# Optimization experiments

Hardware: AMD Instinct MI355X
Metric: run time of the kernel (lower is better)

## Reference

```python
import jax, jax.numpy as jnp
import numpy as np

B, D, C, K = 8192, 2048, 4096, 1000  # batch, input_dim, num_centers, num_classes


def setup_inputs() -> dict:
    key = jax.random.key(0)
    k0, k1, k2 = jax.random.split(key, 3)
    x = jax.random.normal(k0, (B, D), dtype=jnp.float32)
    centers = jax.random.normal(k1, (C, D), dtype=jnp.float32)
    beta = jnp.ones((C,), dtype=jnp.float32)
    W = jax.random.normal(k2, (K, C), dtype=jnp.float32) * 0.02  # fc.weight
    b = jnp.zeros((K,), dtype=jnp.float32)  # fc.bias
    return {"x": x, "centers": centers, "beta": beta, "W": W, "b": b}


def reference(x, centers, beta, W, b):
    # Pairwise Euclidean distance via the Gram trick (same math as
    # torch.norm(x[:,None,:] - centers, dim=2), without the (B,C,D) intermediate).
    x2 = jnp.sum(x * x, axis=-1, keepdims=True)          # (B, 1)
    c2 = jnp.sum(centers * centers, axis=-1)             # (C,)
    sq = x2 + c2[None, :] - 2.0 * (x @ centers.T)        # (B, C) squared distances
    dist = jnp.sqrt(jnp.maximum(sq, 0.0))
    act = jnp.exp(-beta[None, :] * dist)                 # RBF activations
    act = act / jnp.sum(act, axis=1, keepdims=True)      # normalize over centers
    return act @ W.T + b                                 # linear head (B, K)
```

## Files before the change

### kernel.cpp

```cpp
#include <hip/hip_runtime.h>


#define BB 8192
#define DD 2048
#define CC 4096
#define KK 1000
#define KP 1024

typedef unsigned short u16;
typedef __bf16 bf16x8 __attribute__((ext_vector_type(8)));
typedef float f32x4 __attribute__((ext_vector_type(4)));

typedef const void __attribute__((address_space(1)))* gvp_t;
typedef void __attribute__((address_space(3)))* lvp_t;

__device__ __forceinline__ u16 f2bf(float f) {
  union { float f; unsigned u; } v; v.f = f;
  return (u16)((v.u + 0x7fffu + ((v.u >> 16) & 1u)) >> 16);
}

__global__ void prep_all(const float* __restrict__ x, const float* __restrict__ cen,
                         const float* __restrict__ W,
                         u16* __restrict__ xb, u16* __restrict__ cb,
                         u16* __restrict__ wb,
                         float* __restrict__ x2, float* __restrict__ c2) {
  int row = blockIdx.x;
  int t = threadIdx.x;
  if (row >= BB + CC) {
    int r = row - BB - CC;
    ushort4* dst = reinterpret_cast<ushort4*>(wb + (size_t)r * CC);
    if (r < KK) {
      const float4* src = reinterpret_cast<const float4*>(W + (size_t)r * CC);
#pragma unroll
      for (int m = 0; m < 4; ++m) {
        float4 v = src[t + 256 * m];
        dst[t + 256 * m] = make_ushort4(f2bf(v.x), f2bf(v.y), f2bf(v.z), f2bf(v.w));
      }
    } else {
#pragma unroll
      for (int m = 0; m < 4; ++m) dst[t + 256 * m] = make_ushort4(0, 0, 0, 0);
    }
    return;
  }
  const float* src;
  u16* dst;
  float* nrm;
  if (row < BB) {
    src = x + (size_t)row * DD; dst = xb + (size_t)row * DD; nrm = x2 + row;
  } else {
    int r = row - BB;
    src = cen + (size_t)r * DD; dst = cb + (size_t)r * DD; nrm = c2 + r;
  }
  float s = 0.f;
#pragma unroll
  for (int m = 0; m < 2; ++m) {
    int idx = t + 256 * m;
    float4 v = reinterpret_cast<const float4*>(src)[idx];
    s += v.x * v.x + v.y * v.y + v.z * v.z + v.w * v.w;
    reinterpret_cast<ushort4*>(dst)[idx] =
        make_ushort4(f2bf(v.x), f2bf(v.y), f2bf(v.z), f2bf(v.w));
  }
#pragma unroll
  for (int off = 1; off < 64; off <<= 1) s += __shfl_xor(s, off);
  __shared__ float red[4];
  if ((t & 63) == 0) red[t >> 6] = s;
  __syncthreads();
  if (t == 0) *nrm = red[0] + red[1] + red[2] + red[3];
}

#define SB0 __builtin_amdgcn_sched_barrier(0)
#define BARR __builtin_amdgcn_s_barrier()
#define LGKM0 asm volatile("s_waitcnt lgkmcnt(0)" ::: "memory")


#define ST_A(BUF, H, TILE)                                                         \
  {                                                                                \
    const u16* _s = gA0 + (size_t)((H) * 128) * DD + (TILE) * 64;                  \
    char* _d = (char*)smem + (BUF) * 65536 + (H) * 16384 + t * 16;                 \
    __builtin_amdgcn_global_load_lds((gvp_t)_s, (lvp_t)_d, 16, 0, 0);              \
    __builtin_amdgcn_global_load_lds((gvp_t)(_s + (size_t)64 * DD),                \
                                     (lvp_t)(_d + 8192), 16, 0, 0);                \
  }

#define ST_B(BUF, H, TILE)                                                         \
  {                                                                                \
    const u16* _s = gB0 + (size_t)((H) * 128) * DD + (TILE) * 64;                  \
    char* _d = (char*)smem + (BUF) * 65536 + 32768 + (H) * 16384 + t * 16;         \
    __builtin_amdgcn_global_load_lds((gvp_t)_s, (lvp_t)_d, 16, 0, 0);              \
    __builtin_amdgcn_global_load_lds((gvp_t)(_s + (size_t)64 * DD),                \
                                     (lvp_t)(_d + 8192), 16, 0, 0);                \
  }

#define READ_B(SBP)                                                                \
  _Pragma("unroll") for (int n_ = 0; n_ < 4; ++n_) {                               \
    _Pragma("unroll") for (int ks_ = 0; ks_ < 2; ++ks_) {                          \
      bfr[n_][ks_] = *(const bf16x8*)((SBP) + bRow + n_ * 2048 + cbv[ks_]);        \
    }                                                                              \
  }

#define READ_A(SAP, MQ)                                                            \
  _Pragma("unroll") for (int m_ = 0; m_ < 2; ++m_) {                               \
    _Pragma("unroll") for (int ks_ = 0; ks_ < 2; ++ks_) {                          \
      af[m_][ks_] =                                                                \
          *(const bf16x8*)((SAP) + aRow + ((MQ)*2 + m_) * 2048 + cbv[ks_]);        \
    }                                                                              \
  }

#define MFMA_Q(MQ)                                                                 \
  __builtin_amdgcn_s_setprio(1);                                                   \
  _Pragma("unroll") for (int m_ = 0; m_ < 2; ++m_) {                               \
    _Pragma("unroll") for (int n_ = 0; n_ < 4; ++n_) {                             \
      _Pragma("unroll") for (int ks_ = 0; ks_ < 2; ++ks_) {                        \
        acc[(MQ)*2 + m_][n_] = __builtin_amdgcn_mfma_f32_16x16x32_bf16(            \
            af[m_][ks_], bfr[n_][ks_], acc[(MQ)*2 + m_][n_], 0, 0, 0);             \
      }                                                                            \
    }                                                                              \
  }                                                                                \
  __builtin_amdgcn_s_setprio(0)

#define TILE_BODY(TILE, CUR, DOA, DOB, VMN)                                        \
  {                                                                                \
    const char* sA_ = (const char*)smem + (CUR) * 65536;                           \
    const char* sB_ = sA_ + 32768;                                                 \
    READ_B(sB_);                                                                   \
    READ_A(sA_, 0);                                                                \
    SB0;                                                                           \
    if (DOA) { ST_A(1 - (CUR), 0, (TILE) + 1); ST_A(1 - (CUR), 1, (TILE) + 1); }   \
    SB0; LGKM0; SB0;                                                               \
    MFMA_Q(0); SB0; BARR;                                                          \
    READ_A(sA_, 1); SB0;                                                           \
    if (DOB) { ST_B((CUR), 0, (TILE) + 2); }                                       \
    SB0; LGKM0; SB0;                                                               \
    MFMA_Q(1); SB0;                                                                \
    READ_A(sA_, 2); SB0;                                                           \
    if (DOB) { ST_B((CUR), 1, (TILE) + 2); }                                       \
    SB0; LGKM0; SB0;                                                               \
    MFMA_Q(2); SB0;                                                                \
    READ_A(sA_, 3); SB0; LGKM0; SB0;                                               \
    MFMA_Q(3);                                                                     \
    if ((VMN) == 4) { asm volatile("s_waitcnt vmcnt(4)" ::: "memory"); }           \
    else if ((VMN) == 0) { asm volatile("s_waitcnt vmcnt(0)" ::: "memory"); }      \
    SB0; BARR;                                                                     \
  }

__global__ __launch_bounds__(512, 2)
void gemm1_rbf(const u16* __restrict__ Abf, const u16* __restrict__ Bbf,
               const float* __restrict__ x2, const float* __restrict__ c2,
               const float* __restrict__ beta, u16* __restrict__ Ebf,
               float* __restrict__ psum) {
  constexpr int NT = DD / 64;
  __shared__ __align__(16) char smem[131072];

  const int t = threadIdx.x;
  const int lane = t & 63;
  const int wave = t >> 6;
  const int wr = wave >> 2;
  const int wc = wave & 3;
  const int l15 = lane & 15;

  const int rowBase = blockIdx.y * 256;
  const int colBase = blockIdx.x * 256;

  f32x4 acc[8][4];
#pragma unroll
  for (int i = 0; i < 8; ++i)
#pragma unroll
    for (int j = 0; j < 4; ++j) acc[i][j] = 0.f;

  const int srow = t >> 3;
  const u16* gA0 = Abf + (size_t)(rowBase + srow) * DD + ((t & 7) ^ (srow & 7)) * 8;
  const u16* gB0 = Bbf + (size_t)(colBase + srow) * DD + ((t & 7) ^ (srow & 7)) * 8;

  int cbv[2];
  cbv[0] = (((lane >> 4) & 3) ^ (lane & 7)) << 4;
  cbv[1] = ((4 + ((lane >> 4) & 3)) ^ (lane & 7)) << 4;
  const int aRow = (wr * 128 + l15) * 128;
  const int bRow = (wc * 64 + l15) * 128;

  bf16x8 bfr[4][2];
  bf16x8 af[2][2];

  ST_A(0, 0, 0); ST_A(0, 1, 0); ST_B(0, 0, 0); ST_B(0, 1, 0);
  ST_B(1, 0, 1); ST_B(1, 1, 1);
  asm volatile("s_waitcnt vmcnt(4)" ::: "memory");
  BARR;

#pragma unroll 2
  for (int tile = 0; tile < NT - 2; ++tile) {
    TILE_BODY(tile, tile & 1, true, true, 4);
  }
  TILE_BODY(NT - 2, (NT - 2) & 1, true, false, 0);
  TILE_BODY(NT - 1, (NT - 1) & 1, false, false, -1);

  const int khi4 = (lane >> 4) * 4;
  float* lrs = (float*)smem;
  float c2v[4], bet[4];
  int gc[4];
#pragma unroll
  for (int n = 0; n < 4; ++n) {
    gc[n] = colBase + wc * 64 + n * 16 + l15;
    c2v[n] = c2[gc[n]];
    bet[n] = beta[gc[n]];
  }
#pragma unroll
  for (int m = 0; m < 8; ++m) {
#pragma unroll
    for (int r = 0; r < 4; ++r) {
      const int rrel = wr * 128 + m * 16 + khi4 + r;
      const int grow = rowBase + rrel;
      const float x2v = x2[grow];
      u16* orow = Ebf + (size_t)grow * CC;
      float rs = 0.f;
#pragma unroll
      for (int n = 0; n < 4; ++n) {
        float d = acc[m][n][r];
        float sq = fmaxf(x2v + c2v[n] - 2.0f * d, 0.0f);
        float e = __expf(-bet[n] * __builtin_amdgcn_sqrtf(sq));
        rs += e;
        orow[gc[n]] = f2bf(e);
      }
      lrs[rrel * 68 + wc * 16 + l15] = rs;
    }
  }
  __syncthreads();
  if (t < 256) {
    const f32x4* p = (const f32x4*)(lrs + t * 68);
    float s = 0.f;
#pragma unroll
    for (int i = 0; i < 16; ++i) {
      f32x4 v = p[i];
      s += v[0] + v[1] + v[2] + v[3];
    }
    psum[(size_t)blockIdx.x * BB + rowBase + t] = s;
  }
}

__global__ void rowsum_reduce(const float* __restrict__ psum, float* __restrict__ rowsum) {
  const int row = blockIdx.x * 256 + threadIdx.x;
  float s = 0.f;
#pragma unroll
  for (int b = 0; b < 16; ++b) s += psum[(size_t)b * BB + row];
  rowsum[row] = s;
}


#define ST2_A(BUF, H, TILE)                                                        \
  {                                                                                \
    const u16* _s = gA0 + (size_t)((H) * 128) * CC + (TILE) * 64;                  \
    char* _d = (char*)smem + (BUF) * 49152 + (H) * 16384 + t * 16;                 \
    __builtin_amdgcn_global_load_lds((gvp_t)_s, (lvp_t)_d, 16, 0, 0);              \
    __builtin_amdgcn_global_load_lds((gvp_t)(_s + (size_t)64 * CC),                \
                                     (lvp_t)(_d + 8192), 16, 0, 0);                \
  }

#define ST2_B(BUF, TILE)                                                           \
  {                                                                                \
    const u16* _s = gB0 + (TILE) * 64;                                             \
    char* _d = (char*)smem + (BUF) * 49152 + 32768 + t * 16;                       \
    __builtin_amdgcn_global_load_lds((gvp_t)_s, (lvp_t)_d, 16, 0, 0);              \
    __builtin_amdgcn_global_load_lds((gvp_t)(_s + (size_t)64 * CC),                \
                                     (lvp_t)(_d + 8192), 16, 0, 0);                \
  }

#define READ2_B(SBP)                                                               \
  _Pragma("unroll") for (int n_ = 0; n_ < 2; ++n_) {                               \
    _Pragma("unroll") for (int ks_ = 0; ks_ < 2; ++ks_) {                          \
      bfr[n_][ks_] = *(const bf16x8*)((SBP) + bRow + n_ * 2048 + cbv[ks_]);        \
    }                                                                              \
  }

#define READ2_A(SAP, MQ)                                                           \
  _Pragma("unroll") for (int m_ = 0; m_ < 2; ++m_) {                               \
    _Pragma("unroll") for (int ks_ = 0; ks_ < 2; ++ks_) {                          \
      af[m_][ks_] =                                                                \
          *(const bf16x8*)((SAP) + aRow + ((MQ)*2 + m_) * 2048 + cbv[ks_]);        \
    }                                                                              \
  }

#define MFMA2_Q(MQ)                                                                \
  __builtin_amdgcn_s_setprio(1);                                                   \
  _Pragma("unroll") for (int m_ = 0; m_ < 2; ++m_) {                               \
    _Pragma("unroll") for (int n_ = 0; n_ < 2; ++n_) {                             \
      _Pragma("unroll") for (int ks_ = 0; ks_ < 2; ++ks_) {                        \
        acc[(MQ)*2 + m_][n_] = __builtin_amdgcn_mfma_f32_16x16x32_bf16(            \
            af[m_][ks_], bfr[n_][ks_], acc[(MQ)*2 + m_][n_], 0, 0, 0);             \
      }                                                                            \
    }                                                                              \
  }                                                                                \
  __builtin_amdgcn_s_setprio(0)

#define TILE2_BODY(TILE, CUR, DOA, DOB, VMN)                                       \
  {                                                                                \
    const char* sA_ = (const char*)smem + (CUR) * 49152;                           \
    const char* sB_ = sA_ + 32768;                                                 \
    READ2_B(sB_);                                                                  \
    READ2_A(sA_, 0);                                                               \
    SB0;                                                                           \
    if (DOA) { ST2_A(1 - (CUR), 0, (TILE) + 1); }                                  \
    SB0; LGKM0; SB0;                                                               \
    MFMA2_Q(0); SB0; BARR;                                                         \
    READ2_A(sA_, 1); SB0;                                                          \
    if (DOA) { ST2_A(1 - (CUR), 1, (TILE) + 1); }                                  \
    SB0; LGKM0; SB0;                                                               \
    MFMA2_Q(1); SB0;                                                               \
    READ2_A(sA_, 2); SB0;                                                          \
    if (DOB) { ST2_B((CUR), (TILE) + 2); }                                         \
    SB0; LGKM0; SB0;                                                               \
    MFMA2_Q(2); SB0;                                                               \
    READ2_A(sA_, 3); SB0; LGKM0; SB0;                                              \
    MFMA2_Q(3);                                                                    \
    if ((VMN) == 2) { asm volatile("s_waitcnt vmcnt(2)" ::: "memory"); }           \
    else if ((VMN) == 0) { asm volatile("s_waitcnt vmcnt(0)" ::: "memory"); }      \
    SB0; BARR;                                                                     \
  }

__global__ __launch_bounds__(512, 2)
void gemm2_out(const u16* __restrict__ Ebf, const u16* __restrict__ Wbf,
               const float* __restrict__ rowsum, const float* __restrict__ bias,
               float* __restrict__ out) {
  constexpr int NT = CC / 64;
  __shared__ __align__(16) char smem[98304];

  const int t = threadIdx.x;
  const int lane = t & 63;
  const int wave = t >> 6;
  const int wr = wave >> 2;
  const int wc = wave & 3;
  const int l15 = lane & 15;

  const int d = blockIdx.x + (blockIdx.y << 3);
  const int s_ = d >> 3;
  const int by = (d & 7) + ((s_ >> 3) << 3);
  const int bx = s_ & 7;

  const int rowBase = by * 256;
  const int colBase = bx * 128;

  f32x4 acc[8][2];
#pragma unroll
  for (int i = 0; i < 8; ++i)
#pragma unroll
    for (int j = 0; j < 2; ++j) acc[i][j] = 0.f;

  const int srow = t >> 3;
  const u16* gA0 = Ebf + (size_t)(rowBase + srow) * CC + ((t & 7) ^ (srow & 7)) * 8;
  const u16* gB0 = Wbf + (size_t)(colBase + srow) * CC + ((t & 7) ^ (srow & 7)) * 8;

  int cbv[2];
  cbv[0] = (((lane >> 4) & 3) ^ (lane & 7)) << 4;
  cbv[1] = ((4 + ((lane >> 4) & 3)) ^ (lane & 7)) << 4;
  const int aRow = (wr * 128 + l15) * 128;
  const int bRow = (wc * 32 + l15) * 128;

  bf16x8 bfr[2][2];
  bf16x8 af[2][2];

  ST2_A(0, 0, 0); ST2_A(0, 1, 0); ST2_B(0, 0);
  ST2_B(1, 1);
  asm volatile("s_waitcnt vmcnt(2)" ::: "memory");
  BARR;

#pragma unroll 2
  for (int tile = 0; tile < NT - 2; ++tile) {
    TILE2_BODY(tile, tile & 1, true, true, 2);
  }
  TILE2_BODY(NT - 2, (NT - 2) & 1, true, false, 0);
  TILE2_BODY(NT - 1, (NT - 1) & 1, false, false, -1);

  const int khi4 = (lane >> 4) * 4;
  int gc[2];
  float bv[2];
#pragma unroll
  for (int n = 0; n < 2; ++n) {
    gc[n] = colBase + wc * 32 + n * 16 + l15;
    bv[n] = (gc[n] < KK) ? bias[gc[n]] : 0.f;
  }
#pragma unroll
  for (int m = 0; m < 8; ++m) {
#pragma unroll
    for (int r = 0; r < 4; ++r) {
      const int grow = rowBase + wr * 128 + m * 16 + khi4 + r;
      const float inv = 1.0f / rowsum[grow];
#pragma unroll
      for (int n = 0; n < 2; ++n) {
        if (gc[n] < KK)
          out[(size_t)grow * KK + gc[n]] = acc[m][n][r] * inv + bv[n];
      }
    }
  }
}

#define OFF_XB 0u
#define OFF_CB 33554432u
#define OFF_WB 50331648u
#define OFF_EB 58720256u
#define OFF_X2 125829120u
#define OFF_C2 125861888u
#define OFF_RS 125878272u

extern "C" void kernel_launch(void* const* d_in, const int* in_sizes, int n_in,
                              void* d_out, int out_size, void* d_ws, size_t ws_size,
                              hipStream_t stream) {
  const float* x = (const float*)d_in[0];
  const float* cen = (const float*)d_in[1];
  const float* beta = (const float*)d_in[2];
  const float* W = (const float*)d_in[3];
  const float* bias = (const float*)d_in[4];
  float* out = (float*)d_out;
  char* ws = (char*)d_ws;

  u16* xb = (u16*)(ws + OFF_XB);
  u16* cb = (u16*)(ws + OFF_CB);
  u16* wb = (u16*)(ws + OFF_WB);
  u16* eb = (u16*)(ws + OFF_EB);
  float* x2 = (float*)(ws + OFF_X2);
  float* c2 = (float*)(ws + OFF_C2);
  float* rowsum = (float*)(ws + OFF_RS);
  float* psum = out;

  prep_all<<<BB + CC + KP, 256, 0, stream>>>(x, cen, W, xb, cb, wb, x2, c2);
  gemm1_rbf<<<dim3(CC / 256, BB / 256), 512, 0, stream>>>(xb, cb, x2, c2, beta, eb, psum);
  rowsum_reduce<<<BB / 256, 256, 0, stream>>>(psum, rowsum);
  gemm2_out<<<dim3(KP / 128, BB / 256), 512, 0, stream>>>(eb, wb, rowsum, bias, out);
}
```

Measured before the change: 337.6 us.

## Simplify GEMM prefetch to one-tile-ahead and double-buffer A fragments

Both GEMM main loops are restructured. Previously, B tiles were prefetched two tiles ahead into the current buffer, which needed a barrier in the middle of each tile. Now A and B for the next tile are issued together at the start of each tile into the other buffer, leaving one barrier per tile. A fragment reads are ping-ponged between two register sets so the next quarter's LDS reads overlap the current quarter's MFMAs. The trade-off is a shorter prefetch distance for B, a full vmcnt(0) wait at the end of every tile, and more VGPR usage.

```diff
diff --git a/kernel.cpp b/kernel.cpp
--- a/kernel.cpp
+++ b/kernel.cpp
@@ -71,6 +71,7 @@
 #define SB0 __builtin_amdgcn_sched_barrier(0)
 #define BARR __builtin_amdgcn_s_barrier()
 #define LGKM0 asm volatile("s_waitcnt lgkmcnt(0)" ::: "memory")
+#define VM0 asm volatile("s_waitcnt vmcnt(0)" ::: "memory")
 
 
 #define ST_A(BUF, H, TILE)                                                         \
@@ -98,48 +99,46 @@
     }                                                                              \
   }
 
-#define READ_A(SAP, MQ)                                                            \
+#define READ_AF(DST, SAP, MQ)                                                      \
   _Pragma("unroll") for (int m_ = 0; m_ < 2; ++m_) {                               \
     _Pragma("unroll") for (int ks_ = 0; ks_ < 2; ++ks_) {                          \
-      af[m_][ks_] =                                                                \
+      DST[m_][ks_] =                                                               \
           *(const bf16x8*)((SAP) + aRow + ((MQ)*2 + m_) * 2048 + cbv[ks_]);        \
     }                                                                              \
   }
 
-#define MFMA_Q(MQ)                                                                 \
+#define MFMA_QF(SRC, MQ)                                                           \
   __builtin_amdgcn_s_setprio(1);                                                   \
   _Pragma("unroll") for (int m_ = 0; m_ < 2; ++m_) {                               \
     _Pragma("unroll") for (int n_ = 0; n_ < 4; ++n_) {                             \
       _Pragma("unroll") for (int ks_ = 0; ks_ < 2; ++ks_) {                        \
         acc[(MQ)*2 + m_][n_] = __builtin_amdgcn_mfma_f32_16x16x32_bf16(            \
-            af[m_][ks_], bfr[n_][ks_], acc[(MQ)*2 + m_][n_], 0, 0, 0);             \
+            SRC[m_][ks_], bfr[n_][ks_], acc[(MQ)*2 + m_][n_], 0, 0, 0);            \
       }                                                                            \
     }                                                                              \
   }                                                                                \
   __builtin_amdgcn_s_setprio(0)
 
-#define TILE_BODY(TILE, CUR, DOA, DOB, VMN)                                        \
+#define TILE_BODY(TILE, CUR, DOS)                                                  \
   {                                                                                \
     const char* sA_ = (const char*)smem + (CUR) * 65536;                           \
     const char* sB_ = sA_ + 32768;                                                 \
     READ_B(sB_);                                                                   \
-    READ_A(sA_, 0);                                                                \
+    READ_AF(af0, sA_, 0);                                                          \
     SB0;                                                                           \
-    if (DOA) { ST_A(1 - (CUR), 0, (TILE) + 1); ST_A(1 - (CUR), 1, (TILE) + 1); }   \
+    if (DOS) {                                                                     \
+      ST_A(1 - (CUR), 0, (TILE) + 1); ST_A(1 - (CUR), 1, (TILE) + 1);              \
+      ST_B(1 - (CUR), 0, (TILE) + 1); ST_B(1 - (CUR), 1, (TILE) + 1);              \
+    }                                                                              \
     SB0; LGKM0; SB0;                                                               \
-    MFMA_Q(0); SB0; BARR;                                                          \
-    READ_A(sA_, 1); SB0;                                                           \
-    if (DOB) { ST_B((CUR), 0, (TILE) + 2); }                                       \
-    SB0; LGKM0; SB0;                                                               \
-    MFMA_Q(1); SB0;                                                                \
-    READ_A(sA_, 2); SB0;                                                           \
-    if (DOB) { ST_B((CUR), 1, (TILE) + 2); }                                       \
-    SB0; LGKM0; SB0;                                                               \
-    MFMA_Q(2); SB0;                                                                \
-    READ_A(sA_, 3); SB0; LGKM0; SB0;                                               \
-    MFMA_Q(3);                                                                     \
-    if ((VMN) == 4) { asm volatile("s_waitcnt vmcnt(4)" ::: "memory"); }           \
-    else if ((VMN) == 0) { asm volatile("s_waitcnt vmcnt(0)" ::: "memory"); }      \
+    READ_AF(af1, sA_, 1); SB0;                                                     \
+    MFMA_QF(af0, 0); SB0; LGKM0; SB0;                                              \
+    READ_AF(af0, sA_, 2); SB0;                                                     \
+    MFMA_QF(af1, 1); SB0; LGKM0; SB0;                                              \
+    READ_AF(af1, sA_, 3); SB0;                                                     \
+    MFMA_QF(af0, 2); SB0; LGKM0; SB0;                                              \
+    MFMA_QF(af1, 3);                                                               \
+    if (DOS) { VM0; }                                                              \
     SB0; BARR;                                                                     \
   }
 
@@ -178,19 +177,17 @@
   const int bRow = (wc * 64 + l15) * 128;
 
   bf16x8 bfr[4][2];
-  bf16x8 af[2][2];
+  bf16x8 af0[2][2], af1[2][2];
 
   ST_A(0, 0, 0); ST_A(0, 1, 0); ST_B(0, 0, 0); ST_B(0, 1, 0);
-  ST_B(1, 0, 1); ST_B(1, 1, 1);
-  asm volatile("s_waitcnt vmcnt(4)" ::: "memory");
+  VM0;
   BARR;
 
 #pragma unroll 2
-  for (int tile = 0; tile < NT - 2; ++tile) {
-    TILE_BODY(tile, tile & 1, true, true, 4);
-  }
-  TILE_BODY(NT - 2, (NT - 2) & 1, true, false, 0);
-  TILE_BODY(NT - 1, (NT - 1) & 1, false, false, -1);
+  for (int tile = 0; tile < NT - 1; ++tile) {
+    TILE_BODY(tile, tile & 1, true);
+  }
+  TILE_BODY(NT - 1, (NT - 1) & 1, false);
 
   const int khi4 = (lane >> 4) * 4;
   float* lrs = (float*)smem;
@@ -269,48 +266,46 @@
     }                                                                              \
   }
 
-#define READ2_A(SAP, MQ)                                                           \
+#define READ2_AF(DST, SAP, MQ)                                                     \
   _Pragma("unroll") for (int m_ = 0; m_ < 2; ++m_) {                               \
     _Pragma("unroll") for (int ks_ = 0; ks_ < 2; ++ks_) {                          \
-      af[m_][ks_] =                                                                \
+      DST[m_][ks_] =                                                               \
           *(const bf16x8*)((SAP) + aRow + ((MQ)*2 + m_) * 2048 + cbv[ks_]);        \
     }                                                                              \
   }
 
-#define MFMA2_Q(MQ)                                                                \
+#define MFMA2_QF(SRC, MQ)                                                          \
   __builtin_amdgcn_s_setprio(1);                                                   \
   _Pragma("unroll") for (int m_ = 0; m_ < 2; ++m_) {                               \
     _Pragma("unroll") for (int n_ = 0; n_ < 2; ++n_) {                             \
       _Pragma("unroll") for (int ks_ = 0; ks_ < 2; ++ks_) {                        \
         acc[(MQ)*2 + m_][n_] = __builtin_amdgcn_mfma_f32_16x16x32_bf16(            \
-            af[m_][ks_], bfr[n_][ks_], acc[(MQ)*2 + m_][n_], 0, 0, 0);             \
+            SRC[m_][ks_], bfr[n_][ks_], acc[(MQ)*2 + m_][n_], 0, 0, 0);            \
       }                                                                            \
     }                                                                              \
   }                                                                                \
   __builtin_amdgcn_s_setprio(0)
 
-#define TILE2_BODY(TILE, CUR, DOA, DOB, VMN)                                       \
+#define TILE2_BODY(TILE, CUR, DOS)                                                 \
   {                                                                                \
     const char* sA_ = (const char*)smem + (CUR) * 49152;                           \
     const char* sB_ = sA_ + 32768;                                                 \
     READ2_B(sB_);                                                                  \
-    READ2_A(sA_, 0);                                                               \
+    READ2_AF(af0, sA_, 0);                                                         \
     SB0;                                                                           \
-    if (DOA) { ST2_A(1 - (CUR), 0, (TILE) + 1); }                                  \
+    if (DOS) {                                                                     \
+      ST2_A(1 - (CUR), 0, (TILE) + 1); ST2_A(1 - (CUR), 1, (TILE) + 1);            \
+      ST2_B(1 - (CUR), (TILE) + 1);                                                \
+    }                                                                              \
     SB0; LGKM0; SB0;                                                               \
-    MFMA2_Q(0); SB0; BARR;                                                         \
-    READ2_A(sA_, 1); SB0;                                                          \
-    if (DOA) { ST2_A(1 - (CUR), 1, (TILE) + 1); }                                  \
-    SB0; LGKM0; SB0;                                                               \
-    MFMA2_Q(1); SB0;                                                               \
-    READ2_A(sA_, 2); SB0;                                                          \
-    if (DOB) { ST2_B((CUR), (TILE) + 2); }                                         \
-    SB0; LGKM0; SB0;                                                               \
-    MFMA2_Q(2); SB0;                                                               \
-    READ2_A(sA_, 3); SB0; LGKM0; SB0;                                              \
-    MFMA2_Q(3);                                                                    \
-    if ((VMN) == 2) { asm volatile("s_waitcnt vmcnt(2)" ::: "memory"); }           \
-    else if ((VMN) == 0) { asm volatile("s_waitcnt vmcnt(0)" ::: "memory"); }      \
+    READ2_AF(af1, sA_, 1); SB0;                                                    \
+    MFMA2_QF(af0, 0); SB0; LGKM0; SB0;                                             \
+    READ2_AF(af0, sA_, 2); SB0;                                                    \
+    MFMA2_QF(af1, 1); SB0; LGKM0; SB0;                                             \
+    READ2_AF(af1, sA_, 3); SB0;                                                    \
+    MFMA2_QF(af0, 2); SB0; LGKM0; SB0;                                             \
+    MFMA2_QF(af1, 3);                                                              \
+    if (DOS) { VM0; }                                                              \
     SB0; BARR;                                                                     \
   }
 
@@ -353,19 +348,17 @@
   const int bRow = (wc * 32 + l15) * 128;
 
   bf16x8 bfr[2][2];
-  bf16x8 af[2][2];
+  bf16x8 af0[2][2], af1[2][2];
 
   ST2_A(0, 0, 0); ST2_A(0, 1, 0); ST2_B(0, 0);
-  ST2_B(1, 1);
-  asm volatile("s_waitcnt vmcnt(2)" ::: "memory");
+  VM0;
   BARR;
 
 #pragma unroll 2
-  for (int tile = 0; tile < NT - 2; ++tile) {
-    TILE2_BODY(tile, tile & 1, true, true, 2);
-  }
-  TILE2_BODY(NT - 2, (NT - 2) & 1, true, false, 0);
-  TILE2_BODY(NT - 1, (NT - 1) & 1, false, false, -1);
+  for (int tile = 0; tile < NT - 1; ++tile) {
+    TILE2_BODY(tile, tile & 1, true);
+  }
+  TILE2_BODY(NT - 1, (NT - 1) & 1, false);
 
   const int khi4 = (lane >> 4) * 4;
   int gc[2];
```

New measurement: 342.3 us. No clear change (+1.4%).

## Restructure gemm1 LDS pipeline and fold the row-sum reduction into gemm2

Applied to the files above, without the earlier changes.

The gemm1 tile loop now reads all four A fragment groups from LDS up front into separate register arrays. It prefetches both the A and B halves of the next tile into the other buffer in one batch, and uses partial lgkmcnt(8) waits so MFMAs can start before every LDS read has landed. This removes the previous two-tile-ahead B prefetch, so each tile ends with a full vmcnt(0) wait, and it raises register pressure. Separately, the rowsum_reduce kernel is removed: gemm2 reads the 16 partial sums for its 256 rows at startup and keeps them in LDS, saving one launch and a global round trip. The partial sums live inside the output buffer that gemm2 also writes, so correctness relies on every block reading them before any block writes over that region.

```diff
diff --git a/kernel.cpp b/kernel.cpp
--- a/kernel.cpp
+++ b/kernel.cpp
@@ -71,6 +71,8 @@
 #define SB0 __builtin_amdgcn_sched_barrier(0)
 #define BARR __builtin_amdgcn_s_barrier()
 #define LGKM0 asm volatile("s_waitcnt lgkmcnt(0)" ::: "memory")
+#define LGKM8 asm volatile("s_waitcnt lgkmcnt(8)" ::: "memory")
+#define VM0 asm volatile("s_waitcnt vmcnt(0)" ::: "memory")
 
 
 #define ST_A(BUF, H, TILE)                                                         \
@@ -98,48 +100,46 @@
     }                                                                              \
   }
 
-#define READ_A(SAP, MQ)                                                            \
+#define READ_AF(DST, SAP, MQ)                                                      \
   _Pragma("unroll") for (int m_ = 0; m_ < 2; ++m_) {                               \
     _Pragma("unroll") for (int ks_ = 0; ks_ < 2; ++ks_) {                          \
-      af[m_][ks_] =                                                                \
+      DST[m_][ks_] =                                                               \
           *(const bf16x8*)((SAP) + aRow + ((MQ)*2 + m_) * 2048 + cbv[ks_]);        \
     }                                                                              \
   }
 
-#define MFMA_Q(MQ)                                                                 \
+#define MFMA_QF(SRC, MQ)                                                           \
   __builtin_amdgcn_s_setprio(1);                                                   \
   _Pragma("unroll") for (int m_ = 0; m_ < 2; ++m_) {                               \
     _Pragma("unroll") for (int n_ = 0; n_ < 4; ++n_) {                             \
       _Pragma("unroll") for (int ks_ = 0; ks_ < 2; ++ks_) {                        \
         acc[(MQ)*2 + m_][n_] = __builtin_amdgcn_mfma_f32_16x16x32_bf16(            \
-            af[m_][ks_], bfr[n_][ks_], acc[(MQ)*2 + m_][n_], 0, 0, 0);             \
+            SRC[m_][ks_], bfr[n_][ks_], acc[(MQ)*2 + m_][n_], 0, 0, 0);            \
       }                                                                            \
     }                                                                              \
   }                                                                                \
   __builtin_amdgcn_s_setprio(0)
 
-#define TILE_BODY(TILE, CUR, DOA, DOB, VMN)                                        \
+#define TILE_BODY(TILE, CUR, DOS)                                                  \
   {                                                                                \
     const char* sA_ = (const char*)smem + (CUR) * 65536;                           \
     const char* sB_ = sA_ + 32768;                                                 \
     READ_B(sB_);                                                                   \
-    READ_A(sA_, 0);                                                                \
+    READ_AF(af0, sA_, 0);                                                          \
+    READ_AF(af1, sA_, 1);                                                          \
     SB0;                                                                           \
-    if (DOA) { ST_A(1 - (CUR), 0, (TILE) + 1); ST_A(1 - (CUR), 1, (TILE) + 1); }   \
-    SB0; LGKM0; SB0;                                                               \
-    MFMA_Q(0); SB0; BARR;                                                          \
-    READ_A(sA_, 1); SB0;                                                           \
-    if (DOB) { ST_B((CUR), 0, (TILE) + 2); }                                       \
-    SB0; LGKM0; SB0;                                                               \
-    MFMA_Q(1); SB0;                                                                \
-    READ_A(sA_, 2); SB0;                                                           \
-    if (DOB) { ST_B((CUR), 1, (TILE) + 2); }                                       \
-    SB0; LGKM0; SB0;                                                               \
-    MFMA_Q(2); SB0;                                                                \
-    READ_A(sA_, 3); SB0; LGKM0; SB0;                                               \
-    MFMA_Q(3);                                                                     \
-    if ((VMN) == 4) { asm volatile("s_waitcnt vmcnt(4)" ::: "memory"); }           \
-    else if ((VMN) == 0) { asm volatile("s_waitcnt vmcnt(0)" ::: "memory"); }      \
+    if (DOS) {                                                                     \
+      ST_A(1 - (CUR), 0, (TILE) + 1); ST_A(1 - (CUR), 1, (TILE) + 1);              \
+      ST_B(1 - (CUR), 0, (TILE) + 1); ST_B(1 - (CUR), 1, (TILE) + 1);              \
+    }                                                                              \
+    SB0; LGKM8; SB0;                               \
+    READ_AF(af2, sA_, 2); SB0;                                                     \
+    MFMA_QF(af0, 0); SB0; LGKM8; SB0;                \
+    READ_AF(af3, sA_, 3); SB0;                                                     \
+    MFMA_QF(af1, 1); SB0; LGKM8; SB0;                \
+    MFMA_QF(af2, 2); SB0; LGKM0; SB0;                               \
+    MFMA_QF(af3, 3);                                                               \
+    if (DOS) { VM0; }                                                              \
     SB0; BARR;                                                                     \
   }
 
@@ -178,19 +178,17 @@
   const int bRow = (wc * 64 + l15) * 128;
 
   bf16x8 bfr[4][2];
-  bf16x8 af[2][2];
+  bf16x8 af0[2][2], af1[2][2], af2[2][2], af3[2][2];
 
   ST_A(0, 0, 0); ST_A(0, 1, 0); ST_B(0, 0, 0); ST_B(0, 1, 0);
-  ST_B(1, 0, 1); ST_B(1, 1, 1);
-  asm volatile("s_waitcnt vmcnt(4)" ::: "memory");
+  VM0;
   BARR;
 
 #pragma unroll 2
-  for (int tile = 0; tile < NT - 2; ++tile) {
-    TILE_BODY(tile, tile & 1, true, true, 4);
-  }
-  TILE_BODY(NT - 2, (NT - 2) & 1, true, false, 0);
-  TILE_BODY(NT - 1, (NT - 1) & 1, false, false, -1);
+  for (int tile = 0; tile < NT - 1; ++tile) {
+    TILE_BODY(tile, tile & 1, true);
+  }
+  TILE_BODY(NT - 1, (NT - 1) & 1, false);
 
   const int khi4 = (lane >> 4) * 4;
   float* lrs = (float*)smem;
@@ -233,14 +231,6 @@
     }
     psum[(size_t)blockIdx.x * BB + rowBase + t] = s;
   }
-}
-
-__global__ void rowsum_reduce(const float* __restrict__ psum, float* __restrict__ rowsum) {
-  const int row = blockIdx.x * 256 + threadIdx.x;
-  float s = 0.f;
-#pragma unroll
-  for (int b = 0; b < 16; ++b) s += psum[(size_t)b * BB + row];
-  rowsum[row] = s;
 }
 
 
@@ -316,10 +306,11 @@
 
 __global__ __launch_bounds__(512, 2)
 void gemm2_out(const u16* __restrict__ Ebf, const u16* __restrict__ Wbf,
-               const float* __restrict__ rowsum, const float* __restrict__ bias,
+               const float* psum, const float* __restrict__ bias,
                float* __restrict__ out) {
   constexpr int NT = CC / 64;
   __shared__ __align__(16) char smem[98304];
+  __shared__ float rsum_lds[256];
 
   const int t = threadIdx.x;
   const int lane = t & 63;
@@ -355,8 +346,15 @@
   bf16x8 bfr[2][2];
   bf16x8 af[2][2];
 
+  float rsv = 0.f;
+  if (t < 256) {
+#pragma unroll
+    for (int b = 0; b < 16; ++b) rsv += psum[(size_t)b * BB + rowBase + t];
+  }
+
   ST2_A(0, 0, 0); ST2_A(0, 1, 0); ST2_B(0, 0);
   ST2_B(1, 1);
+  if (t < 256) rsum_lds[t] = rsv;
   asm volatile("s_waitcnt vmcnt(2)" ::: "memory");
   BARR;
 
@@ -379,8 +377,9 @@
   for (int m = 0; m < 8; ++m) {
 #pragma unroll
     for (int r = 0; r < 4; ++r) {
-      const int grow = rowBase + wr * 128 + m * 16 + khi4 + r;
-      const float inv = 1.0f / rowsum[grow];
+      const int rrel = wr * 128 + m * 16 + khi4 + r;
+      const int grow = rowBase + rrel;
+      const float inv = 1.0f / rsum_lds[rrel];
 #pragma unroll
       for (int n = 0; n < 2; ++n) {
         if (gc[n] < KK)
@@ -396,7 +395,6 @@
 #define OFF_EB 58720256u
 #define OFF_X2 125829120u
 #define OFF_C2 125861888u
-#define OFF_RS 125878272u
 
 extern "C" void kernel_launch(void* const* d_in, const int* in_sizes, int n_in,
                               void* d_out, int out_size, void* d_ws, size_t ws_size,
@@ -415,11 +413,9 @@
   u16* eb = (u16*)(ws + OFF_EB);
   float* x2 = (float*)(ws + OFF_X2);
   float* c2 = (float*)(ws + OFF_C2);
-  float* rowsum = (float*)(ws + OFF_RS);
   float* psum = out;
 
   prep_all<<<BB + CC + KP, 256, 0, stream>>>(x, cen, W, xb, cb, wb, x2, c2);
   gemm1_rbf<<<dim3(CC / 256, BB / 256), 512, 0, stream>>>(xb, cb, x2, c2, beta, eb, psum);
-  rowsum_reduce<<<BB / 256, 256, 0, stream>>>(psum, rowsum);
-  gemm2_out<<<dim3(KP / 128, BB / 256), 512, 0, stream>>>(eb, wb, rowsum, bias, out);
+  gemm2_out<<<dim3(KP / 128, BB / 256), 512, 0, stream>>>(eb, wb, psum, bias, out);
 }
```

New measurement: 341.4 us. No clear change (+1.1%).
